# Kernel optimization log

Measured on AMD Instinct MI355X. Metric: run time of the kernel, lower is better.

Reference implementation:

```python
import jax, jax.numpy as jnp
import numpy as np

K = 20
EPS = 1e-5


def knn_idx(x, k):
    # x: (B,C,N); returns indices of k nearest neighbors (largest negative sq dist)
    xx = jnp.sum(x * x, axis=1)                       # (B,N)
    inner = jnp.einsum('bcn,bcm->bnm', x, x)          # (B,N,N)
    dist = 2.0 * inner - xx[:, :, None] - xx[:, None, :]
    return jax.lax.top_k(dist, k)[1]                  # (B,N,k)


def gather_nb(x, idx):
    # x: (B,C,N), idx: (B,N,k) -> (B,N,k,C)
    xt = jnp.transpose(x, (0, 2, 1))
    return jax.vmap(lambda t, i: t[i])(xt, idx)


def bn(x, g, b, m, v):
    # eval-mode batchnorm over channel axis 1
    sh = [1] * x.ndim
    sh[1] = -1
    inv = g / jnp.sqrt(v + EPS)
    return (x - m.reshape(sh)) * inv.reshape(sh) + b.reshape(sh)


def graph_feature(x, k=K):
    # x: (B,C,N) -> (B,3C,N,k): [neighbor, center, center-neighbor]
    idx = knn_idx(x, k)
    nb = gather_nb(x, idx)                            # (B,N,k,C)
    ctr = jnp.broadcast_to(jnp.transpose(x, (0, 2, 1))[:, :, None, :], nb.shape)
    f = jnp.concatenate([nb, ctr, ctr - nb], axis=-1)
    return jnp.transpose(f, (0, 3, 1, 2))


def att_pool(x, g, b, m, v, W, wb):
    # x: (B,C,N,k); BN->ReLU->1x1 conv -> softmax over k -> weighted sum
    h = jax.nn.relu(bn(x, g, b, m, v))
    act = jnp.einsum('bcnk,oc->bonk', h, W) + wb[None, :, None, None]
    scores = jax.nn.softmax(act, axis=-1)
    return jnp.sum(x * scores, axis=-1)               # (B,C,N)


def lafe(x, W1, b1, W2, b2, W3, b3):
    # local attention extraction; x: (B,3,N) -> (B,16,N)
    idx = knn_idx(x, K)
    nb = gather_nb(x, idx)                            # (B,N,k,3)
    ctr = jnp.broadcast_to(jnp.transpose(x, (0, 2, 1))[:, :, None, :], nb.shape)
    x_n = ctr - nb
    new_f = jnp.einsum('bnkc,oc->bnko', ctr, W1) + b1
    self_att = jnp.einsum('bnko,o->bnk', new_f, W3[0]) + b3[0]
    edge = jnp.einsum('bnkc,oc->bnko', x_n, W2) + b2  # (B,N,k,16)
    nb_att = jnp.einsum('bnko,o->bnk', edge, W3[0]) + b3[0]
    logits = self_att + nb_att                        # (B,N,k)
    coefs = jax.nn.softmax(jax.nn.leaky_relu(logits, 0.01), axis=-1)
    vals = jnp.einsum('bnk,bnko->bno', coefs, edge)   # (B,N,16)
    return jnp.transpose(jax.nn.elu(vals), (0, 2, 1))


def _forward(x, law1, lab1, law2, lab2, law3, lab3,
             mlp_w, mlp_b, mlp_g, mlp_be, mlp_m, mlp_v,
             c1_w, bn1_g, bn1_b, bn1_m, bn1_v,
             p1_g, p1_b, p1_m, p1_v, p1_w, p1_wb,
             c2_w, bn2_g, bn2_b, bn2_m, bn2_v,
             p2_g, p2_b, p2_m, p2_v, p2_w, p2_wb,
             c3_w, bn3_g, bn3_b, bn3_m, bn3_v):
    xm = lafe(x, law1, lab1, law2, lab2, law3, lab3)          # (B,16,N)
    x_manet = jnp.concatenate([x, xm], axis=1)                # (B,19,N)
    x_mlp = jax.nn.relu(bn(jnp.einsum('bcn,oc->bon', x_manet, mlp_w) + mlp_b[None, :, None],
                           mlp_g, mlp_be, mlp_m, mlp_v))      # (B,256,N)
    g = graph_feature(x_manet)                                # (B,57,N,k)
    h1 = jax.nn.leaky_relu(bn(jnp.einsum('bcnk,oc->bonk', g, c1_w),
                              bn1_g, bn1_b, bn1_m, bn1_v), 0.2)
    x_p1 = att_pool(h1, p1_g, p1_b, p1_m, p1_v, p1_w, p1_wb)  # (B,64,N)
    x_c1 = jnp.concatenate([x_manet, x_p1], axis=1)           # (B,83,N)
    g2 = graph_feature(x_c1)                                  # (B,249,N,k)
    h2 = jax.nn.leaky_relu(bn(jnp.einsum('bcnk,oc->bonk', g2, c2_w),
                              bn2_g, bn2_b, bn2_m, bn2_v), 0.2)
    x_p2 = att_pool(h2, p2_g, p2_b, p2_m, p2_v, p2_w, p2_wb)  # (B,256,N)
    x_c2 = jnp.concatenate([x_mlp, x_p2], axis=1)             # (B,512,N)
    return jax.nn.leaky_relu(bn(jnp.einsum('bcn,oc->bon', x_c2, c3_w),
                                bn3_g, bn3_b, bn3_m, bn3_v), 0.2)


def setup_inputs() -> dict:
    key = jax.random.key(0)
    ks = iter(jax.random.split(key, 16))
    f32 = jnp.float32
    def W(*s):
        return jax.random.normal(next(ks), s, f32) * 0.05
    B, N = 8, 2048
    def bn_params(c):
        return jnp.ones((c,), f32), jnp.zeros((c,), f32), jnp.zeros((c,), f32), jnp.ones((c,), f32)
    d = {}
    d['x'] = jax.random.normal(next(ks), (B, 3, N), f32)
    d['law1'], d['lab1'] = W(16, 3), jnp.zeros((16,), f32)
    d['law2'], d['lab2'] = W(16, 3), jnp.zeros((16,), f32)
    d['law3'], d['lab3'] = W(1, 16), jnp.zeros((1,), f32)
    d['mlp_w'], d['mlp_b'] = W(256, 19), jnp.zeros((256,), f32)
    d['mlp_g'], d['mlp_be'], d['mlp_m'], d['mlp_v'] = bn_params(256)
    d['c1_w'] = W(64, 57)
    d['bn1_g'], d['bn1_b'], d['bn1_m'], d['bn1_v'] = bn_params(64)
    d['p1_g'], d['p1_b'], d['p1_m'], d['p1_v'] = bn_params(64)
    d['p1_w'], d['p1_wb'] = W(64, 64), jnp.zeros((64,), f32)
    d['c2_w'] = W(256, 249)
    d['bn2_g'], d['bn2_b'], d['bn2_m'], d['bn2_v'] = bn_params(256)
    d['p2_g'], d['p2_b'], d['p2_m'], d['p2_v'] = bn_params(256)
    d['p2_w'], d['p2_wb'] = W(256, 256), jnp.zeros((256,), f32)
    d['c3_w'] = W(512, 512)
    d['bn3_g'], d['bn3_b'], d['bn3_m'], d['bn3_v'] = bn_params(512)
    return d


def reference(x, law1, lab1, law2, lab2, law3, lab3,
              mlp_w, mlp_b, mlp_g, mlp_be, mlp_m, mlp_v,
              c1_w, bn1_g, bn1_b, bn1_m, bn1_v,
              p1_g, p1_b, p1_m, p1_v, p1_w, p1_wb,
              c2_w, bn2_g, bn2_b, bn2_m, bn2_v,
              p2_g, p2_b, p2_m, p2_v, p2_w, p2_wb,
              c3_w, bn3_g, bn3_b, bn3_m, bn3_v):
    return _forward(x, law1, lab1, law2, lab2, law3, lab3,
                    mlp_w, mlp_b, mlp_g, mlp_be, mlp_m, mlp_v,
                    c1_w, bn1_g, bn1_b, bn1_m, bn1_v,
                    p1_g, p1_b, p1_m, p1_v, p1_w, p1_wb,
                    c2_w, bn2_g, bn2_b, bn2_m, bn2_v,
                    p2_g, p2_b, p2_m, p2_v, p2_w, p2_wb,
                    c3_w, bn3_g, bn3_b, bn3_m, bn3_v)
```

## Files before the change

kernel.cpp:

```cpp
#include <hip/hip_runtime.h>
#include <math.h>
#include <float.h>

#define NB 8
#define NP 2048
#define KNN 20
#define BN_EPS 1e-5f

typedef __attribute__((ext_vector_type(8))) short short8v;
typedef __attribute__((ext_vector_type(4))) float f32x4;
typedef __attribute__((ext_vector_type(16))) float f32x16;

__device__ __forceinline__ float leakyf(float x, float s) { return x >= 0.f ? x : s * x; }

__device__ __forceinline__ unsigned short f2bf(float f) {
  unsigned u = __float_as_uint(f);
  u = u + 0x7fffu + ((u >> 16) & 1u);
  return (unsigned short)(u >> 16);
}
__device__ __forceinline__ float bf2f(unsigned short h) {
  return __uint_as_float((unsigned)h << 16);
}
__device__ __forceinline__ unsigned sortkey(float f) {
  unsigned u = __float_as_uint(f);
  return (u & 0x80000000u) ? ~u : (u | 0x80000000u);
}

__global__ void copy_ch_k(const float* __restrict__ src, int srcC,
                          float* __restrict__ dst, int dstC, int row0, int nch) {
  int i = blockIdx.x * 256 + threadIdx.x;
  int total = NB * nch * NP;
  if (i < total) {
    int n = i & (NP - 1); int t = i >> 11; int c = t % nch; int b = t / nch;
    dst[((size_t)b * dstC + row0 + c) * NP + n] = src[((size_t)b * srcC + c) * NP + n];
  }
}

__global__ void xx_k(const float* __restrict__ src, int C, float* __restrict__ xx) {
  int i = blockIdx.x * 256 + threadIdx.x;
  if (i < NB * NP) {
    int n = i & (NP - 1); int b = i >> 11;
    const float* xb = src + (size_t)b * C * NP + n;
    float s = 0.f;
    for (int c = 0; c < C; ++c) { float v = xb[(size_t)c * NP]; s += v * v; }
    xx[i] = s;
  }
}

__global__ void prepall_k(const float* __restrict__ c1w, const float* __restrict__ mlpw,
                          const float* __restrict__ p1w, const float* __restrict__ c2w,
                          const float* __restrict__ p2w, const float* __restrict__ c3w,
                          const float* g2, const float* b2, const float* m2, const float* v2,
                          const float* pg, const float* pb, const float* pm, const float* pv,
                          const float* g3, const float* b3, const float* m3, const float* v3,
                          float* __restrict__ wn1t, float* __restrict__ wc1t,
                          float* __restrict__ mlp_wt, float* __restrict__ p1_wt,
                          unsigned short* __restrict__ Wnc, unsigned short* __restrict__ p2wB,
                          unsigned short* __restrict__ W3p,
                          float* __restrict__ fold2, float* __restrict__ fold3) {
  int i = blockIdx.x * 256 + threadIdx.x;
  if (i < 19 * 64) {
    int c = i >> 6, o = i & 63;
    float wd = c1w[o * 57 + 38 + c];
    wn1t[i] = c1w[o * 57 + c] - wd;
    wc1t[i] = c1w[o * 57 + 19 + c] + wd;
    return;
  }
  i -= 19 * 64;
  if (i < 19 * 256) {
    int o = i / 19, c = i - o * 19;
    mlp_wt[c * 256 + o] = mlpw[i];
    return;
  }
  i -= 19 * 256;
  if (i < 64 * 64) {
    int o = i >> 6, c = i & 63;
    p1_wt[c * 64 + o] = p1w[i];
    return;
  }
  i -= 64 * 64;
  if (i < 256 * 192) {
    int o = i / 192, c = i - o * 192;
    unsigned short v = 0;
    if (c < 83) v = f2bf(c2w[o * 249 + c] - c2w[o * 249 + 166 + c]);
    else if (c >= 96 && c < 96 + 83) {
      int cc = c - 96;
      v = f2bf(c2w[o * 249 + 83 + cc] + c2w[o * 249 + 166 + cc]);
    }
    Wnc[i] = v;
    return;
  }
  i -= 256 * 192;
  if (i < 256 * 256) { p2wB[i] = f2bf(p2w[i]); return; }
  i -= 256 * 256;
  if (i < 512 * 1024) {
    int o = i >> 10, k = i & 1023;
    W3p[i] = f2bf(c3w[o * 512 + (k & 511)]);
    return;
  }
  i -= 512 * 1024;
  if (i < 256) {
    int o = i;
    float s2 = g2[o] / sqrtf(v2[o] + BN_EPS);
    fold2[o] = s2; fold2[256 + o] = b2[o] - m2[o] * s2;
    float sp = pg[o] / sqrtf(pv[o] + BN_EPS);
    fold2[512 + o] = sp; fold2[768 + o] = pb[o] - pm[o] * sp;
    return;
  }
  i -= 256;
  if (i < 512) {
    int o = i;
    float s = g3[o] / sqrtf(v3[o] + BN_EPS);
    fold3[o] = s;
    fold3[512 + o] = b3[o] - m3[o] * s;
  }
}
#define PREPALL_TOTAL (19*64 + 19*256 + 64*64 + 256*192 + 256*256 + 512*1024 + 256 + 512)

__global__ void packall_k(const unsigned short* __restrict__ Wnc,
                          const unsigned short* __restrict__ p2wB,
                          unsigned short* __restrict__ pw1, unsigned short* __restrict__ pw2) {
  int i = blockIdx.x * 256 + threadIdx.x;
  if (i < 8 * 12 * 64) {
    int lane = i & 63, ks = (i >> 6) % 12, ot = i / (64 * 12);
    int o = ot * 32 + (lane & 31), c = ks * 16 + 8 * (lane >> 5);
#pragma unroll
    for (int e = 0; e < 8; ++e) pw1[i * 8 + e] = Wnc[(size_t)o * 192 + c + e];
    return;
  }
  int j = i - 8 * 12 * 64;
  if (j < 8 * 16 * 64) {
    int lane = j & 63, ks = (j >> 6) % 16, ot = j / (64 * 16);
    int o = ot * 32 + (lane & 31), c = ks * 16 + 8 * (lane >> 5);
#pragma unroll
    for (int e = 0; e < 8; ++e) pw2[j * 8 + e] = p2wB[(size_t)o * 256 + c + e];
  }
}

#define DKC 16
__global__ __launch_bounds__(256) void dist_k(const float* __restrict__ src, int C,
                                              const float* __restrict__ xx,
                                              float* __restrict__ D, int b0) {
  __shared__ float sA[DKC][64];
  __shared__ float sB[DKC][64];
  int bz = blockIdx.z; int b = b0 + bz;
  int n0 = blockIdx.x * 64, m0 = blockIdx.y * 64;
  int tid = threadIdx.x;
  int tn = tid >> 4, tm = tid & 15;
  float acc[4][4] = {};
  const float* xb = src + (size_t)b * C * NP;
  for (int k0 = 0; k0 < C; k0 += DKC) {
    for (int t = tid; t < DKC * 64; t += 256) {
      int kk = t >> 6, i = t & 63;
      int c = k0 + kk;
      float a = 0.f, bb = 0.f;
      if (c < C) { a = xb[(size_t)c * NP + n0 + i]; bb = xb[(size_t)c * NP + m0 + i]; }
      sA[kk][i] = a; sB[kk][i] = bb;
    }
    __syncthreads();
#pragma unroll
    for (int kk = 0; kk < DKC; ++kk) {
      float av[4], bv[4];
#pragma unroll
      for (int q = 0; q < 4; ++q) { av[q] = sA[kk][tn * 4 + q]; bv[q] = sB[kk][tm * 4 + q]; }
#pragma unroll
      for (int qi = 0; qi < 4; ++qi)
#pragma unroll
        for (int qj = 0; qj < 4; ++qj) acc[qi][qj] += av[qi] * bv[qj];
    }
    __syncthreads();
  }
  const float* xxb = xx + (size_t)b * NP;
#pragma unroll
  for (int qi = 0; qi < 4; ++qi) {
    int n = n0 + tn * 4 + qi; float xn = xxb[n];
#pragma unroll
    for (int qj = 0; qj < 4; ++qj) {
      int m = m0 + tm * 4 + qj;
      D[((size_t)bz * NP + n) * NP + m] = 2.f * acc[qi][qj] - xn - xxb[m];
    }
  }
}

__global__ __launch_bounds__(64) void topk_k(const float* __restrict__ D,
                                             int* __restrict__ idxo, int rowbase) {
  int row = blockIdx.x;
  const float* d = D + (size_t)row * NP;
  int lane = threadIdx.x;
  float v[32];
#pragma unroll
  for (int j = 0; j < 32; ++j) v[j] = d[lane + 64 * j];
  int* out = idxo + (size_t)(rowbase + row) * KNN;
  for (int it = 0; it < KNN; ++it) {
    float bv = v[0]; int bj = 0;
#pragma unroll
    for (int j = 1; j < 32; ++j) { if (v[j] > bv) { bv = v[j]; bj = j; } }
    int bm = lane + 64 * bj;
    unsigned long long key = ((unsigned long long)sortkey(bv) << 32) | (unsigned)(~bm);
#pragma unroll
    for (int off = 1; off < 64; off <<= 1) {
      unsigned long long ok = __shfl_xor(key, off);
      if (ok > key) key = ok;
    }
    int bmw = ~(unsigned)key;
    if (lane == 0) out[it] = bmw;
    if ((bmw & 63) == lane) v[bmw >> 6] = -FLT_MAX;
  }
}

__global__ __launch_bounds__(64) void lafe_k(const float* __restrict__ x, const int* __restrict__ idx,
                                             const float* __restrict__ W1, const float* __restrict__ b1,
                                             const float* __restrict__ W2, const float* __restrict__ b2,
                                             const float* __restrict__ W3, const float* __restrict__ b3,
                                             float* __restrict__ x_manet) {
  int t = blockIdx.x * 64 + threadIdx.x;
  if (t >= NB * NP) return;
  int b = t >> 11, n = t & (NP - 1);
  const float* xb = x + (size_t)b * 3 * NP;
  float ctr[3];
#pragma unroll
  for (int c = 0; c < 3; ++c) ctr[c] = xb[c * NP + n];
  float self_s = b3[0];
#pragma unroll
  for (int o = 0; o < 16; ++o) {
    float nf = b1[o];
#pragma unroll
    for (int c = 0; c < 3; ++c) nf += ctr[c] * W1[o * 3 + c];
    self_s += nf * W3[o];
  }
  const int* id = idx + (size_t)t * KNN;
  float logit[KNN];
  float mx = -FLT_MAX;
  for (int k = 0; k < KNN; ++k) {
    int j = id[k];
    float xn[3];
#pragma unroll
    for (int c = 0; c < 3; ++c) xn[c] = ctr[c] - xb[c * NP + j];
    float natt = b3[0];
#pragma unroll
    for (int o = 0; o < 16; ++o) {
      float e = b2[o];
#pragma unroll
      for (int c = 0; c < 3; ++c) e += xn[c] * W2[o * 3 + c];
      natt += e * W3[o];
    }
    float lg = self_s + natt;
    lg = leakyf(lg, 0.01f);
    logit[k] = lg; mx = fmaxf(mx, lg);
  }
  float s = 0.f;
#pragma unroll
  for (int k = 0; k < KNN; ++k) { logit[k] = expf(logit[k] - mx); s += logit[k]; }
  float invs = 1.f / s;
  float vals[16] = {};
  for (int k = 0; k < KNN; ++k) {
    int j = id[k];
    float xn[3];
#pragma unroll
    for (int c = 0; c < 3; ++c) xn[c] = ctr[c] - xb[c * NP + j];
    float w = logit[k] * invs;
#pragma unroll
    for (int o = 0; o < 16; ++o) {
      float e = b2[o];
#pragma unroll
      for (int c = 0; c < 3; ++c) e += xn[c] * W2[o * 3 + c];
      vals[o] += w * e;
    }
  }
#pragma unroll
  for (int o = 0; o < 16; ++o) {
    float v = vals[o];
    v = v > 0.f ? v : expm1f(v);
    x_manet[((size_t)b * 19 + 3 + o) * NP + n] = v;
  }
}

__global__ __launch_bounds__(256) void mlp_k(const float* __restrict__ xman, const float* __restrict__ wt,
                                             const float* __restrict__ bias,
                                             const float* __restrict__ g, const float* __restrict__ be,
                                             const float* __restrict__ m, const float* __restrict__ v,
                                             unsigned short* __restrict__ actT) {
  int o0 = (threadIdx.x & 31) * 8;
  int n = blockIdx.x * 8 + (threadIdx.x >> 5);
  int b = blockIdx.z;
  const float* xb = xman + (size_t)b * 19 * NP;
  float acc[8];
#pragma unroll
  for (int q = 0; q < 8; ++q) acc[q] = bias[o0 + q];
  for (int c = 0; c < 19; ++c) {
    float xv = xb[(size_t)c * NP + n];
    const float4* w4 = reinterpret_cast<const float4*>(wt + c * 256 + o0);
    float4 wa = w4[0], wb4 = w4[1];
    float wr[8] = {wa.x, wa.y, wa.z, wa.w, wb4.x, wb4.y, wb4.z, wb4.w};
#pragma unroll
    for (int q = 0; q < 8; ++q) acc[q] += xv * wr[q];
  }
  short8v hi8, lo8;
#pragma unroll
  for (int q = 0; q < 8; ++q) {
    int o = o0 + q;
    float inv = g[o] / sqrtf(v[o] + BN_EPS);
    float z = fmaxf((acc[q] - m[o]) * inv + be[o], 0.f);
    unsigned short h = f2bf(z);
    hi8[q] = (short)h;
    lo8[q] = (short)f2bf(z - bf2f(h));
  }
  size_t base = ((size_t)b * NP + n) * 1024;
  *reinterpret_cast<short8v*>(actT + base + o0) = hi8;
  *reinterpret_cast<short8v*>(actT + base + 512 + o0) = lo8;
}

__global__ __launch_bounds__(256) void hctr1_k(const float* __restrict__ xman,
                                               const float* __restrict__ wc1t,
                                               float* __restrict__ hctr1) {
  int o = threadIdx.x;
  int n = blockIdx.x * 4 + threadIdx.y;
  int b = blockIdx.z;
  const float* xb = xman + (size_t)b * 19 * NP + n;
  float acc = 0.f;
  for (int c = 0; c < 19; ++c) acc += wc1t[c * 64 + o] * xb[(size_t)c * NP];
  hctr1[((size_t)b * 64 + o) * NP + n] = acc;
}

__global__ __launch_bounds__(64, 1) void conv1pool_k(
    const float* __restrict__ xman, const int* __restrict__ idx,
    const float* __restrict__ wn1t, const float* __restrict__ hctr1,
    const float* __restrict__ b1g, const float* __restrict__ b1b,
    const float* __restrict__ b1m, const float* __restrict__ b1v,
    const float* __restrict__ p1g, const float* __restrict__ p1b,
    const float* __restrict__ p1m, const float* __restrict__ p1v,
    const float* __restrict__ p1wt, const float* __restrict__ p1wb,
    float* __restrict__ x_c1) {
  __shared__ __align__(16) float sg[64 * 20];
  __shared__ int jid[KNN];
  int t = blockIdx.x;
  int b = t >> 11, n = t & (NP - 1);
  int lane = threadIdx.x;
  const float* xb = xman + (size_t)b * 19 * NP;
  if (lane < KNN) jid[lane] = idx[(size_t)t * KNN + lane];
  __syncthreads();
  for (int e = lane; e < 19 * KNN; e += 64) {
    int c = e / KNN, k = e - c * KNN;
    sg[c * 20 + k] = xb[(size_t)c * NP + jid[k]];
  }
  __syncthreads();
  float hc = hctr1[((size_t)b * 64 + lane) * NP + n];
  float h[KNN];
#pragma unroll
  for (int k = 0; k < KNN; ++k) h[k] = hc;
  for (int c = 0; c < 19; ++c) {
    float wv = wn1t[c * 64 + lane];
    const float4* gp = reinterpret_cast<const float4*>(sg + c * 20);
    float4 A = gp[0], Bv = gp[1], Cv = gp[2], Dv = gp[3], E = gp[4];
    float gv[20] = {A.x,A.y,A.z,A.w,Bv.x,Bv.y,Bv.z,Bv.w,Cv.x,Cv.y,Cv.z,Cv.w,Dv.x,Dv.y,Dv.z,Dv.w,E.x,E.y,E.z,E.w};
#pragma unroll
    for (int k = 0; k < KNN; ++k) h[k] += wv * gv[k];
  }
  float inv1 = b1g[lane] / sqrtf(b1v[lane] + BN_EPS);
  float m1 = b1m[lane], bb1 = b1b[lane];
  float h1[KNN];
#pragma unroll
  for (int k = 0; k < KNN; ++k) {
    float z = (h[k] - m1) * inv1 + bb1;
    h1[k] = leakyf(z, 0.2f);
  }
  float pinv = p1g[lane] / sqrtf(p1v[lane] + BN_EPS);
  float pm = p1m[lane], pb = p1b[lane];
  __syncthreads();
#pragma unroll
  for (int k = 0; k < KNN; ++k) sg[lane * 20 + k] = fmaxf((h1[k] - pm) * pinv + pb, 0.f);
  __syncthreads();
  float act[KNN] = {};
  for (int c = 0; c < 64; ++c) {
    float wv = p1wt[c * 64 + lane];
    const float4* gp = reinterpret_cast<const float4*>(sg + c * 20);
    float4 A = gp[0], Bv = gp[1], Cv = gp[2], Dv = gp[3], E = gp[4];
    float gv[20] = {A.x,A.y,A.z,A.w,Bv.x,Bv.y,Bv.z,Bv.w,Cv.x,Cv.y,Cv.z,Cv.w,Dv.x,Dv.y,Dv.z,Dv.w,E.x,E.y,E.z,E.w};
#pragma unroll
    for (int k = 0; k < KNN; ++k) act[k] += wv * gv[k];
  }
  float wb = p1wb[lane];
  float mx = -FLT_MAX;
#pragma unroll
  for (int k = 0; k < KNN; ++k) { act[k] += wb; mx = fmaxf(mx, act[k]); }
  float s = 0.f, outv = 0.f;
#pragma unroll
  for (int k = 0; k < KNN; ++k) {
    float e = expf(act[k] - mx);
    s += e; outv += h1[k] * e;
  }
  x_c1[((size_t)b * 83 + 19 + lane) * NP + n] = outv / s;
}

__global__ __launch_bounds__(256) void t2bf_k(const float* __restrict__ xc1,
                                              unsigned short* __restrict__ xc1T) {
  __shared__ unsigned short tile[256 * 96];
  int b = blockIdx.y;
  int n0 = blockIdx.x * 256;
  int tid = threadIdx.x;
  const float* xb = xc1 + (size_t)b * 83 * NP;
  for (int c = 0; c < 83; ++c)
    tile[tid * 96 + c] = f2bf(xb[(size_t)c * NP + n0 + tid]);
#pragma unroll
  for (int c = 83; c < 96; ++c) tile[tid * 96 + c] = 0;
  __syncthreads();
  const float4* src = (const float4*)tile;
  float4* dst = (float4*)(xc1T + ((size_t)b * NP + n0) * 96);
  for (int i = tid; i < 3072; i += 256) dst[i] = src[i];
}

__global__ __launch_bounds__(256, 2) void conv2mfma_k(
    const unsigned short* __restrict__ xc1T, const int* __restrict__ idx,
    const unsigned short* __restrict__ pw1, const unsigned short* __restrict__ pw2,
    const float* __restrict__ fold, unsigned short* __restrict__ actT) {
  __shared__ unsigned short nbF[2 * 6 * 64 * 8];
  __shared__ unsigned short hhF[2 * 16 * 64 * 8];
  __shared__ int jid[64];
  int tid = threadIdx.x;
  int t0 = blockIdx.x * 2;
  int b = t0 >> 11, n0 = t0 & (NP - 1);

  if (tid < 64) {
    int p = tid >> 5, kk = tid & 31;
    int kc = kk < KNN ? kk : KNN - 1;
    jid[tid] = idx[(size_t)(t0 + p) * KNN + kc];
  }
  __syncthreads();
  for (int it = tid; it < 768; it += 256) {
    int p = it >= 384; int rem = it - p * 384;
    int kk = rem / 12, seg = rem - kk * 12;
    int j = jid[p * 32 + kk];
    short8v v = *reinterpret_cast<const short8v*>(xc1T + ((size_t)b * NP + j) * 96 + seg * 8);
    int ks = seg >> 1, hi = seg & 1;
    *reinterpret_cast<short8v*>(&nbF[(((p * 6 + ks) << 6) + hi * 32 + kk) * 8]) = v;
  }
  __syncthreads();

  int w = tid >> 6, l = tid & 63;
  int kk = l & 31, hi = l >> 5;
  int ot0 = w * 2, ot1 = w * 2 + 1;
  const short8v* pw1v = (const short8v*)pw1;
  const short8v* pw2v = (const short8v*)pw2;

  f32x16 acc[2][2];
#pragma unroll
  for (int p = 0; p < 2; ++p)
#pragma unroll
    for (int nt = 0; nt < 2; ++nt)
#pragma unroll
      for (int r = 0; r < 16; ++r) acc[p][nt][r] = 0.f;

#pragma unroll
  for (int ks = 0; ks < 6; ++ks) {
    short8v b0 = pw1v[(ot0 * 12 + ks) * 64 + l];
    short8v b1 = pw1v[(ot1 * 12 + ks) * 64 + l];
    short8v a0 = *reinterpret_cast<const short8v*>(&nbF[((ks << 6) + l) * 8]);
    short8v a1 = *reinterpret_cast<const short8v*>(&nbF[(((6 + ks) << 6) + l) * 8]);
    acc[0][0] = __builtin_amdgcn_mfma_f32_32x32x16_bf16(a0, b0, acc[0][0], 0, 0, 0);
    acc[0][1] = __builtin_amdgcn_mfma_f32_32x32x16_bf16(a0, b1, acc[0][1], 0, 0, 0);
    acc[1][0] = __builtin_amdgcn_mfma_f32_32x32x16_bf16(a1, b0, acc[1][0], 0, 0, 0);
    acc[1][1] = __builtin_amdgcn_mfma_f32_32x32x16_bf16(a1, b1, acc[1][1], 0, 0, 0);
  }
  const unsigned short* ct0 = xc1T + ((size_t)b * NP + n0) * 96 + 8 * hi;
  const unsigned short* ct1 = ct0 + 96;
#pragma unroll
  for (int ks = 0; ks < 6; ++ks) {
    short8v b0 = pw1v[(ot0 * 12 + 6 + ks) * 64 + l];
    short8v b1 = pw1v[(ot1 * 12 + 6 + ks) * 64 + l];
    short8v a0 = *reinterpret_cast<const short8v*>(ct0 + ks * 16);
    short8v a1 = *reinterpret_cast<const short8v*>(ct1 + ks * 16);
    acc[0][0] = __builtin_amdgcn_mfma_f32_32x32x16_bf16(a0, b0, acc[0][0], 0, 0, 0);
    acc[0][1] = __builtin_amdgcn_mfma_f32_32x32x16_bf16(a0, b1, acc[0][1], 0, 0, 0);
    acc[1][0] = __builtin_amdgcn_mfma_f32_32x32x16_bf16(a1, b0, acc[1][0], 0, 0, 0);
    acc[1][1] = __builtin_amdgcn_mfma_f32_32x32x16_bf16(a1, b1, acc[1][1], 0, 0, 0);
  }

#pragma unroll
  for (int p = 0; p < 2; ++p)
#pragma unroll
    for (int nt = 0; nt < 2; ++nt) {
      int o = w * 64 + nt * 32 + kk;
      float s2 = fold[o], o2 = fold[256 + o];
      float sp = fold[512 + o], op = fold[768 + o];
      int cbase = (p * 16 + (o >> 4)) * 64 + ((o >> 3) & 1) * 32;
      int s = (o >> 3) & 3;
#pragma unroll
      for (int r = 0; r < 16; ++r) {
        int row = (r & 3) + 8 * (r >> 2) + 4 * hi;
        float z = leakyf(acc[p][nt][r] * s2 + o2, 0.2f);
        acc[p][nt][r] = z;
        float hh = fmaxf(z * sp + op, 0.f);
        hhF[((cbase + row) ^ s) * 8 + (o & 7)] = f2bf(hh);
      }
    }
  __syncthreads();

  f32x16 acc2[2][2];
#pragma unroll
  for (int p = 0; p < 2; ++p)
#pragma unroll
    for (int nt = 0; nt < 2; ++nt)
#pragma unroll
      for (int r = 0; r < 16; ++r) acc2[p][nt][r] = 0.f;
#pragma unroll
  for (int ks = 0; ks < 16; ++ks) {
    int sr = (l >> 5) | ((ks & 1) << 1);
    short8v b0 = pw2v[(ot0 * 16 + ks) * 64 + l];
    short8v b1 = pw2v[(ot1 * 16 + ks) * 64 + l];
    short8v a0 = *reinterpret_cast<const short8v*>(&hhF[((((ks << 6) + l)) ^ sr) * 8]);
    short8v a1 = *reinterpret_cast<const short8v*>(&hhF[(((((16 + ks) << 6) + l)) ^ sr) * 8]);
    acc2[0][0] = __builtin_amdgcn_mfma_f32_32x32x16_bf16(a0, b0, acc2[0][0], 0, 0, 0);
    acc2[0][1] = __builtin_amdgcn_mfma_f32_32x32x16_bf16(a0, b1, acc2[0][1], 0, 0, 0);
    acc2[1][0] = __builtin_amdgcn_mfma_f32_32x32x16_bf16(a1, b0, acc2[1][0], 0, 0, 0);
    acc2[1][1] = __builtin_amdgcn_mfma_f32_32x32x16_bf16(a1, b1, acc2[1][1], 0, 0, 0);
  }

#pragma unroll
  for (int p = 0; p < 2; ++p) {
    size_t base = ((size_t)b * NP + n0 + p) * 1024;
#pragma unroll
    for (int nt = 0; nt < 2; ++nt) {
      int o = w * 64 + nt * 32 + kk;
      float mx = -FLT_MAX;
#pragma unroll
      for (int r = 0; r < 16; ++r) {
        int row = (r & 3) + 8 * (r >> 2) + 4 * hi;
        if (row < KNN) mx = fmaxf(mx, acc2[p][nt][r]);
      }
      mx = fmaxf(mx, __shfl_xor(mx, 32));
      float s = 0.f, num = 0.f;
#pragma unroll
      for (int r = 0; r < 16; ++r) {
        int row = (r & 3) + 8 * (r >> 2) + 4 * hi;
        if (row < KNN) {
          float e = __expf(acc2[p][nt][r] - mx);
          s += e; num += e * acc[p][nt][r];
        }
      }
      s += __shfl_xor(s, 32);
      num += __shfl_xor(num, 32);
      if (hi == 0) {
        float z = num / s;
        unsigned short h = f2bf(z);
        actT[base + 256 + o] = h;
        actT[base + 768 + o] = f2bf(z - bf2f(h));
      }
    }
  }
}

__global__ __launch_bounds__(256) void conv3mfma_k(const unsigned short* __restrict__ actT,
                                                   const unsigned short* __restrict__ W3p,
                                                   const float* __restrict__ fold3,
                                                   float* __restrict__ out) {
  __shared__ unsigned short sA[128 * 64];
  __shared__ unsigned short sB[128 * 64];
  int b = blockIdx.z;
  int o0 = blockIdx.x * 128, n0 = blockIdx.y * 128;
  int tid = threadIdx.x;
  int wave = tid >> 6, lane = tid & 63;
  int wr = wave >> 1, wc = wave & 1;
  int lrow = lane & 15, lkb2 = (lane >> 4) * 16, lr4 = (lane >> 4) * 4;

  f32x4 acc[4][4];
#pragma unroll
  for (int mt = 0; mt < 4; ++mt)
#pragma unroll
    for (int nt = 0; nt < 4; ++nt) acc[mt][nt] = (f32x4){0.f, 0.f, 0.f, 0.f};

  for (int k0 = 0; k0 < 1024; k0 += 64) {
    for (int i = tid; i < 2048; i += 256) {
      int half = i >> 10;
      int r = (i >> 3) & 127;
      int ci = i & 7;
      const unsigned short* src = half
          ? (actT + ((size_t)b * NP + n0 + r) * 1024 + k0 + ci * 8)
          : (W3p + (size_t)(o0 + r) * 1024 + k0 + ci * 8);
      short8v vv = *reinterpret_cast<const short8v*>(src);
      int byteoff = (r * 128 + ci * 16) ^ ((r & 7) << 4);
      *reinterpret_cast<short8v*>((char*)(half ? sB : sA) + byteoff) = vv;
    }
    __syncthreads();
#pragma unroll
    for (int ks = 0; ks < 2; ++ks) {
      short8v afr[4], bfr[4];
#pragma unroll
      for (int mt = 0; mt < 4; ++mt) {
        int r = wr * 64 + mt * 16 + lrow;
        afr[mt] = *reinterpret_cast<const short8v*>((char*)sA + ((r * 128 + ks * 64 + lkb2) ^ ((r & 7) << 4)));
      }
#pragma unroll
      for (int nt = 0; nt < 4; ++nt) {
        int r = wc * 64 + nt * 16 + lrow;
        bfr[nt] = *reinterpret_cast<const short8v*>((char*)sB + ((r * 128 + ks * 64 + lkb2) ^ ((r & 7) << 4)));
      }
#pragma unroll
      for (int mt = 0; mt < 4; ++mt)
#pragma unroll
        for (int nt = 0; nt < 4; ++nt)
          acc[mt][nt] = __builtin_amdgcn_mfma_f32_16x16x32_bf16(afr[mt], bfr[nt], acc[mt][nt], 0, 0, 0);
    }
    __syncthreads();
  }
#pragma unroll
  for (int mt = 0; mt < 4; ++mt) {
#pragma unroll
    for (int r = 0; r < 4; ++r) {
      int o = o0 + wr * 64 + mt * 16 + lr4 + r;
      float s3 = fold3[o], b3 = fold3[512 + o];
      float* op = out + ((size_t)b * 512 + o) * NP + n0 + wc * 64 + lrow;
#pragma unroll
      for (int nt = 0; nt < 4; ++nt) {
        float z = acc[mt][nt][r] * s3 + b3;
        op[nt * 16] = leakyf(z, 0.2f);
      }
    }
  }
}

extern "C" void kernel_launch(void* const* d_in, const int* in_sizes, int n_in,
                              void* d_out, int out_size, void* d_ws, size_t ws_size,
                              hipStream_t stream) {
  const float* x     = (const float*)d_in[0];
  const float* law1  = (const float*)d_in[1];
  const float* lab1  = (const float*)d_in[2];
  const float* law2  = (const float*)d_in[3];
  const float* lab2  = (const float*)d_in[4];
  const float* law3  = (const float*)d_in[5];
  const float* lab3  = (const float*)d_in[6];
  const float* mlp_w = (const float*)d_in[7];
  const float* mlp_b = (const float*)d_in[8];
  const float* mlp_g = (const float*)d_in[9];
  const float* mlp_be= (const float*)d_in[10];
  const float* mlp_m = (const float*)d_in[11];
  const float* mlp_v = (const float*)d_in[12];
  const float* c1_w  = (const float*)d_in[13];
  const float* bn1_g = (const float*)d_in[14];
  const float* bn1_b = (const float*)d_in[15];
  const float* bn1_m = (const float*)d_in[16];
  const float* bn1_v = (const float*)d_in[17];
  const float* p1_g  = (const float*)d_in[18];
  const float* p1_b  = (const float*)d_in[19];
  const float* p1_m  = (const float*)d_in[20];
  const float* p1_v  = (const float*)d_in[21];
  const float* p1_w  = (const float*)d_in[22];
  const float* p1_wb = (const float*)d_in[23];
  const float* c2_w  = (const float*)d_in[24];
  const float* bn2_g = (const float*)d_in[25];
  const float* bn2_b = (const float*)d_in[26];
  const float* bn2_m = (const float*)d_in[27];
  const float* bn2_v = (const float*)d_in[28];
  const float* p2_g  = (const float*)d_in[29];
  const float* p2_b  = (const float*)d_in[30];
  const float* p2_m  = (const float*)d_in[31];
  const float* p2_v  = (const float*)d_in[32];
  const float* p2_w  = (const float*)d_in[33];
  const float* p2_wb = (const float*)d_in[34];
  const float* c3_w  = (const float*)d_in[35];
  const float* bn3_g = (const float*)d_in[36];
  const float* bn3_b = (const float*)d_in[37];
  const float* bn3_m = (const float*)d_in[38];
  const float* bn3_v = (const float*)d_in[39];

  char* wsb = (char*)d_ws;
  size_t off = 0;
  auto alloc = [&](size_t elems) -> float* {
    float* p = (float*)(wsb + off);
    off += elems * sizeof(float);
    off = (off + 255) & ~(size_t)255;
    return p;
  };
  float* wn1t   = alloc(19 * 64);
  float* wc1t   = alloc(19 * 64);
  float* mlp_wt = alloc(19 * 256);
  float* p1_wt  = alloc(64 * 64);
  unsigned short* Wnc = (unsigned short*)alloc(256 * 192 / 2);
  unsigned short* p2wB = (unsigned short*)alloc(256 * 256 / 2);
  unsigned short* pw1 = (unsigned short*)alloc(8 * 12 * 64 * 8 / 2);
  unsigned short* pw2 = (unsigned short*)alloc(8 * 16 * 64 * 8 / 2);
  unsigned short* W3p  = (unsigned short*)alloc((size_t)512 * 1024 / 2);
  float* fold2  = alloc(1024);
  float* fold3  = alloc(1024);
  float* xxbuf  = alloc((size_t)NB * NP);
  float* x_manet= alloc((size_t)NB * 19 * NP);
  float* x_c1   = alloc((size_t)NB * 83 * NP);
  float* hctr1  = alloc((size_t)NB * 64 * NP);
  unsigned short* xc1T = (unsigned short*)alloc((size_t)NB * NP * 96 / 2);
  unsigned short* actT = (unsigned short*)alloc((size_t)NB * NP * 1024 / 2);
  int*   idxbuf = (int*)alloc((size_t)NB * NP * KNN);
  float* Dbuf   = (float*)(wsb + off);
  size_t fullD = (size_t)NB * NP * NP * sizeof(float);
  int nbc = (off + fullD <= ws_size) ? NB : 1;

  prepall_k<<<(PREPALL_TOTAL + 255) / 256, 256, 0, stream>>>(
      c1_w, mlp_w, p1_w, c2_w, p2_w, c3_w,
      bn2_g, bn2_b, bn2_m, bn2_v, p2_g, p2_b, p2_m, p2_v,
      bn3_g, bn3_b, bn3_m, bn3_v,
      wn1t, wc1t, mlp_wt, p1_wt, Wnc, p2wB, W3p, fold2, fold3);
  packall_k<<<56, 256, 0, stream>>>(Wnc, p2wB, pw1, pw2);

  auto knn = [&](const float* src, int C) {
    xx_k<<<(NB * NP + 255) / 256, 256, 0, stream>>>(src, C, xxbuf);
    for (int b0 = 0; b0 < NB; b0 += nbc) {
      dist_k<<<dim3(NP / 64, NP / 64, nbc), 256, 0, stream>>>(src, C, xxbuf, Dbuf, b0);
      topk_k<<<nbc * NP, 64, 0, stream>>>(Dbuf, idxbuf, b0 * NP);
    }
  };

  copy_ch_k<<<(NB * 3 * NP + 255) / 256, 256, 0, stream>>>(x, 3, x_manet, 19, 0, 3);

  knn(x, 3);
  lafe_k<<<(NB * NP) / 64, 64, 0, stream>>>(x, idxbuf, law1, lab1, law2, lab2, law3, lab3, x_manet);

  mlp_k<<<dim3(NP / 8, 1, NB), 256, 0, stream>>>(x_manet, mlp_wt, mlp_b, mlp_g, mlp_be, mlp_m, mlp_v, actT);

  knn(x_manet, 19);
  hctr1_k<<<dim3(NP / 4, 1, NB), dim3(64, 4), 0, stream>>>(x_manet, wc1t, hctr1);
  conv1pool_k<<<NB * NP, 64, 0, stream>>>(x_manet, idxbuf, wn1t, hctr1,
                                          bn1_g, bn1_b, bn1_m, bn1_v,
                                          p1_g, p1_b, p1_m, p1_v,
                                          p1_wt, p1_wb, x_c1);
  copy_ch_k<<<(NB * 19 * NP + 255) / 256, 256, 0, stream>>>(x_manet, 19, x_c1, 83, 0, 19);

  knn(x_c1, 83);
  t2bf_k<<<dim3(NP / 256, NB), 256, 0, stream>>>(x_c1, xc1T);
  conv2mfma_k<<<NB * NP / 2, 256, 0, stream>>>(xc1T, idxbuf, pw1, pw2, fold2, actT);

  conv3mfma_k<<<dim3(512 / 128, NP / 128, NB), 256, 0, stream>>>(actT, W3p, fold3,
                                                                 (float*)d_out);
}
```

Baseline: 898.7 us.

## Fuse distance and top-k into one kernel for small-channel kNN stages

```diff
diff --git a/kernel.cpp b/kernel.cpp
--- a/kernel.cpp
+++ b/kernel.cpp
@@ -134,6 +134,61 @@
     int o = ot * 32 + (lane & 31), c = ks * 16 + 8 * (lane >> 5);
 #pragma unroll
     for (int e = 0; e < 8; ++e) pw2[j * 8 + e] = p2wB[(size_t)o * 256 + c + e];
+  }
+}
+
+template<int C, int CH>
+__global__ __launch_bounds__(512) void knnf_k(const float* __restrict__ src,
+                                              const float* __restrict__ xx,
+                                              int* __restrict__ idxo) {
+  __shared__ float sB[C][CH];
+  __shared__ float sXm[NP];
+  int b = blockIdx.y;
+  int n0 = blockIdx.x * 8;
+  int tid = threadIdx.x;
+  int wave = tid >> 6, lane = tid & 63;
+  const float* xb = src + (size_t)b * C * NP;
+  const float* xxb = xx + (size_t)b * NP;
+  for (int t = tid; t < NP; t += 512) sXm[t] = xxb[t];
+  int row = n0 + wave;
+  float rf[C];
+#pragma unroll
+  for (int c = 0; c < C; ++c) rf[c] = xb[(size_t)c * NP + row];
+  float xn = xxb[row];
+  float v[32];
+#pragma unroll
+  for (int ch = 0; ch < NP / CH; ++ch) {
+    __syncthreads();
+    for (int t = tid; t < C * CH; t += 512) {
+      int c = t / CH, m = t - c * CH;
+      sB[c][m] = xb[(size_t)c * NP + ch * CH + m];
+    }
+    __syncthreads();
+#pragma unroll
+    for (int jj = 0; jj < CH / 64; ++jj) {
+      float acc = 0.f;
+#pragma unroll
+      for (int c = 0; c < C; ++c)
+        acc = fmaf(rf[c], sB[c][lane + 64 * jj], acc);
+      int m = ch * CH + 64 * jj + lane;
+      v[ch * (CH / 64) + jj] = 2.f * acc - xn - sXm[m];
+    }
+  }
+  int* out = idxo + ((size_t)b * NP + row) * KNN;
+  for (int it = 0; it < KNN; ++it) {
+    float bv = v[0]; int bj = 0;
+#pragma unroll
+    for (int j = 1; j < 32; ++j) if (v[j] > bv) { bv = v[j]; bj = j; }
+    int bm = lane + 64 * bj;
+    unsigned long long key = ((unsigned long long)sortkey(bv) << 32) | (unsigned)(~bm);
+#pragma unroll
+    for (int off = 1; off < 64; off <<= 1) {
+      unsigned long long ok = __shfl_xor(key, off);
+      if (ok > key) key = ok;
+    }
+    int bmw = ~(unsigned)key;
+    if (lane == 0) out[it] = bmw;
+    if ((bmw & 63) == lane) v[bmw >> 6] = -FLT_MAX;
   }
 }
 
@@ -174,28 +229,32 @@
 #pragma unroll
   for (int qi = 0; qi < 4; ++qi) {
     int n = n0 + tn * 4 + qi; float xn = xxb[n];
-#pragma unroll
-    for (int qj = 0; qj < 4; ++qj) {
-      int m = m0 + tm * 4 + qj;
-      D[((size_t)bz * NP + n) * NP + m] = 2.f * acc[qi][qj] - xn - xxb[m];
-    }
+    float4 dv;
+    dv.x = 2.f * acc[qi][0] - xn - xxb[m0 + tm * 4 + 0];
+    dv.y = 2.f * acc[qi][1] - xn - xxb[m0 + tm * 4 + 1];
+    dv.z = 2.f * acc[qi][2] - xn - xxb[m0 + tm * 4 + 2];
+    dv.w = 2.f * acc[qi][3] - xn - xxb[m0 + tm * 4 + 3];
+    *reinterpret_cast<float4*>(&D[((size_t)bz * NP + n) * NP + m0 + tm * 4]) = dv;
   }
 }
 
 __global__ __launch_bounds__(64) void topk_k(const float* __restrict__ D,
                                              int* __restrict__ idxo, int rowbase) {
   int row = blockIdx.x;
-  const float* d = D + (size_t)row * NP;
+  const float4* d4 = reinterpret_cast<const float4*>(D + (size_t)row * NP);
   int lane = threadIdx.x;
   float v[32];
 #pragma unroll
-  for (int j = 0; j < 32; ++j) v[j] = d[lane + 64 * j];
+  for (int j8 = 0; j8 < 8; ++j8) {
+    float4 q = d4[j8 * 64 + lane];
+    v[j8 * 4 + 0] = q.x; v[j8 * 4 + 1] = q.y; v[j8 * 4 + 2] = q.z; v[j8 * 4 + 3] = q.w;
+  }
   int* out = idxo + (size_t)(rowbase + row) * KNN;
   for (int it = 0; it < KNN; ++it) {
     float bv = v[0]; int bj = 0;
 #pragma unroll
     for (int j = 1; j < 32; ++j) { if (v[j] > bv) { bv = v[j]; bj = j; } }
-    int bm = lane + 64 * bj;
+    int bm = (bj >> 2) * 256 + lane * 4 + (bj & 3);
     unsigned long long key = ((unsigned long long)sortkey(bv) << 32) | (unsigned)(~bm);
 #pragma unroll
     for (int off = 1; off < 64; off <<= 1) {
@@ -204,7 +263,7 @@
     }
     int bmw = ~(unsigned)key;
     if (lane == 0) out[it] = bmw;
-    if ((bmw & 63) == lane) v[bmw >> 6] = -FLT_MAX;
+    if (((bmw >> 2) & 63) == lane) v[(bmw >> 8) * 4 + (bmw & 3)] = -FLT_MAX;
   }
 }
 
@@ -699,22 +758,16 @@
       wn1t, wc1t, mlp_wt, p1_wt, Wnc, p2wB, W3p, fold2, fold3);
   packall_k<<<56, 256, 0, stream>>>(Wnc, p2wB, pw1, pw2);
 
-  auto knn = [&](const float* src, int C) {
-    xx_k<<<(NB * NP + 255) / 256, 256, 0, stream>>>(src, C, xxbuf);
-    for (int b0 = 0; b0 < NB; b0 += nbc) {
-      dist_k<<<dim3(NP / 64, NP / 64, nbc), 256, 0, stream>>>(src, C, xxbuf, Dbuf, b0);
-      topk_k<<<nbc * NP, 64, 0, stream>>>(Dbuf, idxbuf, b0 * NP);
-    }
-  };
-
   copy_ch_k<<<(NB * 3 * NP + 255) / 256, 256, 0, stream>>>(x, 3, x_manet, 19, 0, 3);
 
-  knn(x, 3);
+  xx_k<<<(NB * NP + 255) / 256, 256, 0, stream>>>(x, 3, xxbuf);
+  knnf_k<3, 2048><<<dim3(NP / 8, NB), 512, 0, stream>>>(x, xxbuf, idxbuf);
   lafe_k<<<(NB * NP) / 64, 64, 0, stream>>>(x, idxbuf, law1, lab1, law2, lab2, law3, lab3, x_manet);
 
   mlp_k<<<dim3(NP / 8, 1, NB), 256, 0, stream>>>(x_manet, mlp_wt, mlp_b, mlp_g, mlp_be, mlp_m, mlp_v, actT);
 
-  knn(x_manet, 19);
+  xx_k<<<(NB * NP + 255) / 256, 256, 0, stream>>>(x_manet, 19, xxbuf);
+  knnf_k<19, 512><<<dim3(NP / 8, NB), 512, 0, stream>>>(x_manet, xxbuf, idxbuf);
   hctr1_k<<<dim3(NP / 4, 1, NB), dim3(64, 4), 0, stream>>>(x_manet, wc1t, hctr1);
   conv1pool_k<<<NB * NP, 64, 0, stream>>>(x_manet, idxbuf, wn1t, hctr1,
                                           bn1_g, bn1_b, bn1_m, bn1_v,
@@ -722,7 +775,11 @@
                                           p1_wt, p1_wb, x_c1);
   copy_ch_k<<<(NB * 19 * NP + 255) / 256, 256, 0, stream>>>(x_manet, 19, x_c1, 83, 0, 19);
 
-  knn(x_c1, 83);
+  xx_k<<<(NB * NP + 255) / 256, 256, 0, stream>>>(x_c1, 83, xxbuf);
+  for (int b0 = 0; b0 < NB; b0 += nbc) {
+    dist_k<<<dim3(NP / 64, NP / 64, nbc), 256, 0, stream>>>(x_c1, 83, xxbuf, Dbuf, b0);
+    topk_k<<<nbc * NP, 64, 0, stream>>>(Dbuf, idxbuf, b0 * NP);
+  }
   t2bf_k<<<dim3(NP / 256, NB), 256, 0, stream>>>(x_c1, xc1T);
   conv2mfma_k<<<NB * NP / 2, 256, 0, stream>>>(xc1T, idxbuf, pw1, pw2, fold2, actT);
 
```

Measured after the change: 963.1 us. 7.2% more time.
